# Kernel optimization log

Measured on AMD Instinct MI355X. Metric: run time of the kernel, lower is better.

Reference implementation:

```python
import jax, jax.numpy as jnp
import numpy as np

B, S, HID = 2, 2048, 2048
H, G = 16, 1
D = HID // H  # 128


def setup_inputs() -> dict:
    key = jax.random.key(0)
    ks = jax.random.split(key, 10)
    sc = 0.02
    inp = {
        "hidden_states": jax.random.normal(ks[0], (B, S, HID), jnp.float32),
        # 1 above the diagonal -> masked out (matches torch code: scores += mask * -1e9)
        "causal_mask": jnp.triu(jnp.ones((1, 1, S, S), jnp.float32), k=1),
        "padding_mask": jnp.zeros((B, S), jnp.float32),
        "Wq": jax.random.normal(ks[1], (HID, HID), jnp.float32) * sc,
        "bq": jnp.zeros((HID,), jnp.float32),
        "Wk": jax.random.normal(ks[2], (G * D, HID), jnp.float32) * sc,
        "bk": jnp.zeros((G * D,), jnp.float32),
        "Wv": jax.random.normal(ks[3], (G * D, HID), jnp.float32) * sc,
        "bv": jnp.zeros((G * D,), jnp.float32),
        "Wo": jax.random.normal(ks[4], (HID, HID), jnp.float32) * sc,
        "bo": jnp.zeros((HID,), jnp.float32),
    }
    return inp


def reference(hidden_states, causal_mask, padding_mask, Wq, bq, Wk, bk, Wv, bv, Wo, bo):
    b, s, _ = hidden_states.shape
    q = hidden_states @ Wq.T + bq            # [B,S,HID]
    k = hidden_states @ Wk.T + bk            # [B,S,G*D]
    v = hidden_states @ Wv.T + bv            # [B,S,G*D]
    q = q.reshape(b, s, H, D).transpose(0, 2, 1, 3)   # [B,H,S,D]
    k = k.reshape(b, s, G, D).transpose(0, 2, 1, 3)   # [B,G,S,D]
    v = v.reshape(b, s, G, D).transpose(0, 2, 1, 3)   # [B,G,S,D]
    # broadcast G=1 KV heads against H query heads (exactly what torch.matmul does)
    scores = jnp.matmul(q, jnp.swapaxes(k, -1, -2)) / jnp.sqrt(jnp.float32(D))  # [B,H,S,S]
    scores = scores + causal_mask * (-1e9)
    scores = scores + padding_mask[:, None, None, :] * (-1e9)
    weights = jax.nn.softmax(scores, axis=-1)
    out = jnp.matmul(weights, v)                       # [B,H,S,D]
    out = out.transpose(0, 2, 1, 3).reshape(b, s, H * D)
    return out @ Wo.T + bo
```

## Files before the change

kernel.cpp:

```cpp
#include <hip/hip_runtime.h>
#include <hip/hip_bf16.h>

typedef __attribute__((ext_vector_type(8))) short s8v;
typedef __attribute__((ext_vector_type(4))) float f4v;
typedef __hip_bfloat16 bf16;

#define S_LEN 2048
#define HID_DIM 2048
#define N_HEADS 16
#define HEAD_D 128
#define M_ROWS 4096
#define N_FUSED 2304

#define EXP2F(x) __builtin_amdgcn_exp2f(x)

typedef const __attribute__((address_space(1))) unsigned gu_t;
typedef __attribute__((address_space(3))) unsigned lu_t;

static __device__ inline void gload_lds16(const bf16* g, bf16* l) {
  __builtin_amdgcn_global_load_lds((gu_t*)(const void*)g, (lu_t*)(void*)l, 16, 0, 0);
}

static __device__ inline short f2b_bits(float f) {
  bf16 h = __float2bfloat16(f);
  short u;
  __builtin_memcpy(&u, &h, 2);
  return u;
}
static __device__ inline unsigned pk_bf16(float a, float b) {
  __hip_bfloat162 h2 = __float22bfloat162_rn(float2{a, b});
  unsigned u;
  __builtin_memcpy(&u, &h2, 4);
  return u;
}

struct Cvt5 {
  const float* src[5];
  bf16* dst[5];
  long n8[5];
};

__global__ __launch_bounds__(256) void cvt_f32_bf16(Cvt5 c) {
  long i = (long)blockIdx.x * 256 + threadIdx.x;
#pragma unroll
  for (int s = 0; s < 5; ++s) {
    long n8 = c.n8[s];
    if (i < n8) {
      const float* p = c.src[s] + i * 8;
      float4 f0 = *(const float4*)p;
      float4 f1 = *(const float4*)(p + 4);
      s8v t;
      t[0] = f2b_bits(f0.x); t[1] = f2b_bits(f0.y);
      t[2] = f2b_bits(f0.z); t[3] = f2b_bits(f0.w);
      t[4] = f2b_bits(f1.x); t[5] = f2b_bits(f1.y);
      t[6] = f2b_bits(f1.z); t[7] = f2b_bits(f1.w);
      *(s8v*)(c.dst[s] + i * 8) = t;
      return;
    }
    i -= n8;
  }
}

__global__ __launch_bounds__(256) void gemm_qkv(
    const bf16* __restrict__ A, const bf16* __restrict__ Wf,
    const float* __restrict__ bq, const float* __restrict__ bk,
    const float* __restrict__ bv,
    bf16* __restrict__ qout, bf16* __restrict__ kout, bf16* __restrict__ vtout) {
  __shared__ __align__(16) bf16 As[128 * 64];
  __shared__ __align__(16) bf16 Bs[128 * 64];
  const int t = threadIdx.x;
  const int lane = t & 63, wid = t >> 6;
  const int l15 = lane & 15, quad = lane >> 4;
  const int wm = wid >> 1, wn = wid & 1;
  const int bm = blockIdx.x, bn = blockIdx.y;
  const int lr = lane >> 3;
  const int lc = (lane & 7) * 8;
  f4v acc[4][4] = {};
  for (int kt = 0; kt < HID_DIM / 64; ++kt) {
    __syncthreads();
#pragma unroll
    for (int i = 0; i < 4; ++i) {
      int r0 = wid * 32 + i * 8;
      gload_lds16(&A[(size_t)(bm * 128 + r0 + lr) * HID_DIM + kt * 64 + lc], &As[r0 * 64]);
      gload_lds16(&Wf[(size_t)(bn * 128 + r0 + lr) * HID_DIM + kt * 64 + lc], &Bs[r0 * 64]);
    }
    __syncthreads();
#pragma unroll
    for (int ks = 0; ks < 2; ++ks) {
      s8v af[4], bfr[4];
#pragma unroll
      for (int mi = 0; mi < 4; ++mi)
        af[mi] = *(const s8v*)&As[(wm * 64 + mi * 16 + l15) * 64 + ks * 32 + quad * 8];
#pragma unroll
      for (int ni = 0; ni < 4; ++ni)
        bfr[ni] = *(const s8v*)&Bs[(wn * 64 + ni * 16 + l15) * 64 + ks * 32 + quad * 8];
#pragma unroll
      for (int mi = 0; mi < 4; ++mi)
#pragma unroll
        for (int ni = 0; ni < 4; ++ni)
          acc[mi][ni] = __builtin_amdgcn_mfma_f32_16x16x32_bf16(af[mi], bfr[ni], acc[mi][ni], 0, 0, 0);
    }
  }
  if (bn < 16) {
#pragma unroll
    for (int ni = 0; ni < 4; ++ni) {
      int cl = wn * 64 + ni * 16 + l15;
      float bvv = bq[bn * 128 + cl];
#pragma unroll
      for (int mi = 0; mi < 4; ++mi)
#pragma unroll
        for (int r = 0; r < 4; ++r) {
          int row = bm * 128 + wm * 64 + mi * 16 + quad * 4 + r;
          qout[(size_t)row * HID_DIM + bn * 128 + cl] = __float2bfloat16(acc[mi][ni][r] + bvv);
        }
    }
  } else if (bn == 16) {
#pragma unroll
    for (int ni = 0; ni < 4; ++ni) {
      int cl = wn * 64 + ni * 16 + l15;
      float bvv = bk[cl];
#pragma unroll
      for (int mi = 0; mi < 4; ++mi)
#pragma unroll
        for (int r = 0; r < 4; ++r) {
          int row = bm * 128 + wm * 64 + mi * 16 + quad * 4 + r;
          kout[(size_t)row * HEAD_D + cl] = __float2bfloat16(acc[mi][ni][r] + bvv);
        }
    }
  } else {
#pragma unroll
    for (int ni = 0; ni < 4; ++ni) {
      int cl = wn * 64 + ni * 16 + l15;
      float bvv = bv[cl];
#pragma unroll
      for (int mi = 0; mi < 4; ++mi)
#pragma unroll
        for (int r = 0; r < 4; ++r) {
          int row = bm * 128 + wm * 64 + mi * 16 + quad * 4 + r;
          vtout[(size_t)cl * M_ROWS + row] = __float2bfloat16(acc[mi][ni][r] + bvv);
        }
    }
  }
}

template <bool WBF>
__global__ __launch_bounds__(256) void gemm_o(
    const bf16* __restrict__ A, const void* __restrict__ Wp,
    const float* __restrict__ bias, float* __restrict__ C) {
  __shared__ __align__(16) bf16 As[128 * 64];
  __shared__ __align__(16) bf16 Bs[128 * 64];
  const int t = threadIdx.x;
  const int lane = t & 63, wid = t >> 6;
  const int l15 = lane & 15, quad = lane >> 4;
  const int wm = wid >> 1, wn = wid & 1;
  const int bm = blockIdx.x, bn = blockIdx.y;
  const int lr = lane >> 3;
  const int lc = (lane & 7) * 8;
  f4v acc[4][4] = {};
  for (int kt = 0; kt < HID_DIM / 64; ++kt) {
    __syncthreads();
#pragma unroll
    for (int i = 0; i < 4; ++i) {
      int r0 = wid * 32 + i * 8;
      gload_lds16(&A[(size_t)(bm * 128 + r0 + lr) * HID_DIM + kt * 64 + lc], &As[r0 * 64]);
      if constexpr (WBF) {
        gload_lds16(&((const bf16*)Wp)[(size_t)(bn * 128 + r0 + lr) * HID_DIM + kt * 64 + lc],
                    &Bs[r0 * 64]);
      }
    }
    if constexpr (!WBF) {
#pragma unroll
      for (int i = 0; i < 4; ++i) {
        int idx = t + i * 256;
        int row = idx >> 3, c8 = (idx & 7) * 8;
        const float* s = (const float*)Wp + (size_t)(bn * 128 + row) * HID_DIM + kt * 64 + c8;
        float4 f0 = *(const float4*)s;
        float4 f1 = *(const float4*)(s + 4);
        s8v tmp;
        tmp[0] = f2b_bits(f0.x); tmp[1] = f2b_bits(f0.y);
        tmp[2] = f2b_bits(f0.z); tmp[3] = f2b_bits(f0.w);
        tmp[4] = f2b_bits(f1.x); tmp[5] = f2b_bits(f1.y);
        tmp[6] = f2b_bits(f1.z); tmp[7] = f2b_bits(f1.w);
        *(s8v*)&Bs[row * 64 + c8] = tmp;
      }
    }
    __syncthreads();
#pragma unroll
    for (int ks = 0; ks < 2; ++ks) {
      s8v af[4], bfr[4];
#pragma unroll
      for (int mi = 0; mi < 4; ++mi)
        af[mi] = *(const s8v*)&As[(wm * 64 + mi * 16 + l15) * 64 + ks * 32 + quad * 8];
#pragma unroll
      for (int ni = 0; ni < 4; ++ni)
        bfr[ni] = *(const s8v*)&Bs[(wn * 64 + ni * 16 + l15) * 64 + ks * 32 + quad * 8];
#pragma unroll
      for (int mi = 0; mi < 4; ++mi)
#pragma unroll
        for (int ni = 0; ni < 4; ++ni)
          acc[mi][ni] = __builtin_amdgcn_mfma_f32_16x16x32_bf16(af[mi], bfr[ni], acc[mi][ni], 0, 0, 0);
    }
  }
#pragma unroll
  for (int ni = 0; ni < 4; ++ni) {
    int col = bn * 128 + wn * 64 + ni * 16 + l15;
    float bvv = bias[col];
#pragma unroll
    for (int mi = 0; mi < 4; ++mi)
#pragma unroll
      for (int r = 0; r < 4; ++r) {
        int row = bm * 128 + wm * 64 + mi * 16 + quad * 4 + r;
        C[(size_t)row * HID_DIM + col] = acc[mi][ni][r] + bvv;
      }
  }
}

__global__ __launch_bounds__(512, 2) void attn_fwd(
    const bf16* q, const bf16* __restrict__ k, const bf16* __restrict__ vt,
    bf16* o) {
  constexpr int FS = 528;
  __shared__ __align__(16) bf16 KsF[32 * FS];
  __shared__ __align__(16) bf16 VtF[32 * FS];
  __shared__ __align__(16) bf16 PsF[32 * FS];
  const int t = threadIdx.x;
  const int lane = t & 63, w = t >> 6;
  const int l15 = lane & 15, quad = lane >> 4;
  const int p = blockIdx.x >> 1, b = blockIdx.x & 1;
  const size_t bs = (size_t)b * S_LEN;
  const float scale2 = 0.12754245f;

  for (int cc = 0; cc < 2; ++cc) {
    const int c = cc ? p : (255 - p);
    const int row0 = c * 8;
    const int jt = (c >> 4) + 1;
    const int head = w * 2 + (l15 >> 3);

    s8v qf[4];
#pragma unroll
    for (int ks = 0; ks < 4; ++ks)
      qf[ks] = *(const s8v*)&q[(bs + row0 + (l15 & 7)) * HID_DIM +
                               head * HEAD_D + ks * 32 + quad * 8];

    float mst = -1e30f;
    float lst = 0.f;
    f4v acco[8] = {};

    uint4 kreg[4], vreg[4];
#pragma unroll
    for (int i = 0; i < 4; ++i) {
      int idx = t + i * 512;
      kreg[i] = *(const uint4*)&k[(bs + (idx >> 4)) * HEAD_D + (idx & 15) * 8];
      vreg[i] = *(const uint4*)&vt[(size_t)(idx >> 4) * M_ROWS + bs + (idx & 15) * 8];
    }

    for (int j = 0; j < jt; ++j) {
      __syncthreads();
#pragma unroll
      for (int i = 0; i < 4; ++i) {
        int idx = t + i * 512;
        int krow = idx >> 4, kc = idx & 15;
        *(uint4*)&KsF[(((krow >> 4) << 2) | (kc >> 2)) * FS + ((krow & 15) << 5) + ((kc & 3) << 3)] = kreg[i];
        *(uint4*)&VtF[(((krow >> 4) << 2) | (kc >> 2)) * FS + ((krow & 15) << 5) + ((kc & 3) << 3)] = vreg[i];
      }
      if (j + 1 < jt) {
#pragma unroll
        for (int i = 0; i < 4; ++i) {
          int idx = t + i * 512;
          kreg[i] = *(const uint4*)&k[(bs + (j + 1) * 128 + (idx >> 4)) * HEAD_D + (idx & 15) * 8];
          vreg[i] = *(const uint4*)&vt[(size_t)(idx >> 4) * M_ROWS + bs + (j + 1) * 128 + (idx & 15) * 8];
        }
      }
      __syncthreads();

      f4v accs[8] = {};
#pragma unroll
      for (int ks = 0; ks < 4; ++ks) {
        s8v kf[8];
#pragma unroll
        for (int ni = 0; ni < 8; ++ni)
          kf[ni] = *(const s8v*)&KsF[(ni * 4 + ks) * FS + l15 * 32 + quad * 8];
#pragma unroll
        for (int ni = 0; ni < 8; ++ni)
          accs[ni] = __builtin_amdgcn_mfma_f32_16x16x32_bf16(kf[ni], qf[ks], accs[ni], 0, 0, 0);
      }

      const int mg = row0 + (l15 & 7);
      const bool full = (j * 128 + 127 <= row0);
      float tmax = -1e30f;
#pragma unroll
      for (int ni = 0; ni < 8; ++ni)
#pragma unroll
        for (int r = 0; r < 4; ++r) {
          int ng = j * 128 + ni * 16 + quad * 4 + r;
          float s = accs[ni][r];
          if (!full && ng > mg) s = -1e30f;
          accs[ni][r] = s;
          tmax = fmaxf(tmax, s);
        }
      tmax = fmaxf(tmax, __shfl_xor(tmax, 16, 64));
      tmax = fmaxf(tmax, __shfl_xor(tmax, 32, 64));
      float mnew = fmaxf(mst, tmax);
      float nms = -mnew * scale2;
      float alpha = EXP2F(fmaf(mst, scale2, nms));
      float psum = 0.f;
#pragma unroll
      for (int ni = 0; ni < 8; ++ni) {
        float p0 = EXP2F(fmaf(accs[ni][0], scale2, nms));
        float p1 = EXP2F(fmaf(accs[ni][1], scale2, nms));
        float p2 = EXP2F(fmaf(accs[ni][2], scale2, nms));
        float p3 = EXP2F(fmaf(accs[ni][3], scale2, nms));
        psum += (p0 + p1) + (p2 + p3);
        uint2 packed;
        packed.x = pk_bf16(p0, p1);
        packed.y = pk_bf16(p2, p3);
        *(uint2*)&PsF[(w * 4 + (ni >> 1)) * FS + l15 * 32 + (ni & 1) * 16 + quad * 4] = packed;
      }
      psum += __shfl_xor(psum, 16, 64);
      psum += __shfl_xor(psum, 32, 64);
      lst = lst * alpha + psum;
      mst = mnew;
#pragma unroll
      for (int r = 0; r < 4; ++r) {
        float ar = __shfl(alpha, quad * 4 + r, 64);
#pragma unroll
        for (int di = 0; di < 8; ++di) acco[di][r] *= ar;
      }

#pragma unroll
      for (int ks = 0; ks < 4; ++ks) {
        s8v pf, vf[8];
        pf = *(const s8v*)&PsF[(w * 4 + ks) * FS + l15 * 32 + quad * 8];
#pragma unroll
        for (int di = 0; di < 8; ++di)
          vf[di] = *(const s8v*)&VtF[(di * 4 + ks) * FS + l15 * 32 + quad * 8];
#pragma unroll
        for (int di = 0; di < 8; ++di)
          acco[di] = __builtin_amdgcn_mfma_f32_16x16x32_bf16(pf, vf[di], acco[di], 0, 0, 0);
      }
    }

#pragma unroll
    for (int r = 0; r < 4; ++r) {
      int vmq = quad * 4 + r;
      float lr2 = __shfl(lst, vmq, 64);
      float rinv = 1.0f / lr2;
      size_t row = bs + row0 + (vmq & 7);
      int hd = w * 2 + (vmq >> 3);
#pragma unroll
      for (int di = 0; di < 8; ++di)
        o[row * HID_DIM + hd * HEAD_D + di * 16 + l15] = __float2bfloat16(acco[di][r] * rinv);
    }
  }
}

extern "C" void kernel_launch(void* const* d_in, const int* in_sizes, int n_in,
                              void* d_out, int out_size, void* d_ws, size_t ws_size,
                              hipStream_t stream) {
  const float* hs = (const float*)d_in[0];
  const float* Wq = (const float*)d_in[3];
  const float* bq = (const float*)d_in[4];
  const float* Wk = (const float*)d_in[5];
  const float* bk = (const float*)d_in[6];
  const float* Wv = (const float*)d_in[7];
  const float* bv = (const float*)d_in[8];
  const float* Wo = (const float*)d_in[9];
  const float* bo = (const float*)d_in[10];
  float* out = (float*)d_out;

  bf16* qab = (bf16*)d_ws;
  const bool big_ws = ws_size >= (size_t)25 * 1024 * 1024;
  bf16* wob = (bf16*)((char*)d_ws + (size_t)16 * 1024 * 1024);

  char* ob = (char*)d_out;
  bf16* kb = (bf16*)ob;
  bf16* vtb = (bf16*)(ob + (size_t)1048576);
  bf16* hsb = (bf16*)(ob + (size_t)2097152);
  bf16* wqkvb = (bf16*)(ob + (size_t)18874368);

  Cvt5 c;
  c.src[0] = hs; c.dst[0] = hsb;
  c.n8[0] = (long)M_ROWS * HID_DIM / 8;
  c.src[1] = Wq; c.dst[1] = wqkvb;
  c.n8[1] = (long)HID_DIM * HID_DIM / 8;
  c.src[2] = Wk; c.dst[2] = wqkvb + (size_t)HID_DIM * HID_DIM;
  c.n8[2] = (long)HEAD_D * HID_DIM / 8;
  c.src[3] = Wv; c.dst[3] = wqkvb + (size_t)(HID_DIM + HEAD_D) * HID_DIM;
  c.n8[3] = (long)HEAD_D * HID_DIM / 8;
  c.src[4] = Wo; c.dst[4] = big_ws ? wob : (bf16*)nullptr;
  c.n8[4] = big_ws ? (long)HID_DIM * HID_DIM / 8 : 0;
  long total8 = c.n8[0] + c.n8[1] + c.n8[2] + c.n8[3] + c.n8[4];

  cvt_f32_bf16<<<dim3((unsigned)((total8 + 255) / 256)), dim3(256), 0, stream>>>(c);
  gemm_qkv<<<dim3(M_ROWS / 128, N_FUSED / 128), dim3(256), 0, stream>>>(
      hsb, wqkvb, bq, bk, bv, qab, kb, vtb);
  attn_fwd<<<dim3(256), dim3(512), 0, stream>>>(qab, kb, vtb, qab);
  if (big_ws)
    gemm_o<true><<<dim3(M_ROWS / 128, HID_DIM / 128), dim3(256), 0, stream>>>(qab, wob, bo, out);
  else
    gemm_o<false><<<dim3(M_ROWS / 128, HID_DIM / 128), dim3(256), 0, stream>>>(qab, Wo, bo, out);
}
```

Before: 378.0 us.

## Double-buffer GEMM LDS tiles and swizzle attention LDS fragments

The QKV and output-projection GEMMs now use double-buffered LDS tiles. The next K-tile's global-to-LDS loads are issued before computing on the current tile, with one barrier per iteration, and launch bounds request 2 blocks per CU. The attention kernel applies an XOR swizzle to its K, V and P LDS fragment layout to reduce bank conflicts on the 16-byte reads and writes. This doubles GEMM LDS use to 64KB per block, which may limit occupancy. The fp32-weight path of gemm_o stays single-buffered.

```diff
diff --git a/kernel.cpp b/kernel.cpp
--- a/kernel.cpp
+++ b/kernel.cpp
@@ -33,6 +33,8 @@
   __builtin_memcpy(&u, &h2, 4);
   return u;
 }
+
+static __device__ inline int fswz(int i) { return i ^ (((i >> 6) & 3) << 3); }
 
 struct Cvt5 {
   const float* src[5];
@@ -61,13 +63,105 @@
   }
 }
 
-__global__ __launch_bounds__(256) void gemm_qkv(
+__global__ __launch_bounds__(256, 2) void gemm_qkv(
     const bf16* __restrict__ A, const bf16* __restrict__ Wf,
     const float* __restrict__ bq, const float* __restrict__ bk,
     const float* __restrict__ bv,
     bf16* __restrict__ qout, bf16* __restrict__ kout, bf16* __restrict__ vtout) {
-  __shared__ __align__(16) bf16 As[128 * 64];
-  __shared__ __align__(16) bf16 Bs[128 * 64];
+  __shared__ __align__(16) bf16 As[2][128 * 64];
+  __shared__ __align__(16) bf16 Bs[2][128 * 64];
+  const int t = threadIdx.x;
+  const int lane = t & 63, wid = t >> 6;
+  const int l15 = lane & 15, quad = lane >> 4;
+  const int wm = wid >> 1, wn = wid & 1;
+  const int bm = blockIdx.x, bn = blockIdx.y;
+  const int lr = lane >> 3;
+  const int lc = (lane & 7) * 8;
+  const bf16* Ab = &A[(size_t)(bm * 128 + lr) * HID_DIM + lc];
+  const bf16* Bb = &Wf[(size_t)(bn * 128 + lr) * HID_DIM + lc];
+  f4v acc[4][4] = {};
+#pragma unroll
+  for (int i = 0; i < 4; ++i) {
+    int r0 = wid * 32 + i * 8;
+    gload_lds16(Ab + (size_t)r0 * HID_DIM, &As[0][r0 * 64]);
+    gload_lds16(Bb + (size_t)r0 * HID_DIM, &Bs[0][r0 * 64]);
+  }
+  __syncthreads();
+  for (int kt = 0; kt < HID_DIM / 64; ++kt) {
+    const int cur = kt & 1;
+    if (kt + 1 < HID_DIM / 64) {
+#pragma unroll
+      for (int i = 0; i < 4; ++i) {
+        int r0 = wid * 32 + i * 8;
+        gload_lds16(Ab + (size_t)r0 * HID_DIM + (kt + 1) * 64, &As[cur ^ 1][r0 * 64]);
+        gload_lds16(Bb + (size_t)r0 * HID_DIM + (kt + 1) * 64, &Bs[cur ^ 1][r0 * 64]);
+      }
+    }
+#pragma unroll
+    for (int ks = 0; ks < 2; ++ks) {
+      s8v af[4], bfr[4];
+#pragma unroll
+      for (int mi = 0; mi < 4; ++mi)
+        af[mi] = *(const s8v*)&As[cur][(wm * 64 + mi * 16 + l15) * 64 + ks * 32 + quad * 8];
+#pragma unroll
+      for (int ni = 0; ni < 4; ++ni)
+        bfr[ni] = *(const s8v*)&Bs[cur][(wn * 64 + ni * 16 + l15) * 64 + ks * 32 + quad * 8];
+#pragma unroll
+      for (int mi = 0; mi < 4; ++mi)
+#pragma unroll
+        for (int ni = 0; ni < 4; ++ni)
+          acc[mi][ni] = __builtin_amdgcn_mfma_f32_16x16x32_bf16(af[mi], bfr[ni], acc[mi][ni], 0, 0, 0);
+    }
+    __syncthreads();
+  }
+  if (bn < 16) {
+#pragma unroll
+    for (int ni = 0; ni < 4; ++ni) {
+      int cl = wn * 64 + ni * 16 + l15;
+      float bvv = bq[bn * 128 + cl];
+#pragma unroll
+      for (int mi = 0; mi < 4; ++mi)
+#pragma unroll
+        for (int r = 0; r < 4; ++r) {
+          int row = bm * 128 + wm * 64 + mi * 16 + quad * 4 + r;
+          qout[(size_t)row * HID_DIM + bn * 128 + cl] = __float2bfloat16(acc[mi][ni][r] + bvv);
+        }
+    }
+  } else if (bn == 16) {
+#pragma unroll
+    for (int ni = 0; ni < 4; ++ni) {
+      int cl = wn * 64 + ni * 16 + l15;
+      float bvv = bk[cl];
+#pragma unroll
+      for (int mi = 0; mi < 4; ++mi)
+#pragma unroll
+        for (int r = 0; r < 4; ++r) {
+          int row = bm * 128 + wm * 64 + mi * 16 + quad * 4 + r;
+          kout[(size_t)row * HEAD_D + cl] = __float2bfloat16(acc[mi][ni][r] + bvv);
+        }
+    }
+  } else {
+#pragma unroll
+    for (int ni = 0; ni < 4; ++ni) {
+      int cl = wn * 64 + ni * 16 + l15;
+      float bvv = bv[cl];
+#pragma unroll
+      for (int mi = 0; mi < 4; ++mi)
+#pragma unroll
+        for (int r = 0; r < 4; ++r) {
+          int row = bm * 128 + wm * 64 + mi * 16 + quad * 4 + r;
+          vtout[(size_t)cl * M_ROWS + row] = __float2bfloat16(acc[mi][ni][r] + bvv);
+        }
+    }
+  }
+}
+
+template <bool WBF>
+__global__ __launch_bounds__(256, 2) void gemm_o(
+    const bf16* __restrict__ A, const void* __restrict__ Wp,
+    const float* __restrict__ bias, float* __restrict__ C) {
+  __shared__ __align__(16) bf16 As[2][128 * 64];
+  __shared__ __align__(16) bf16 Bs[2][128 * 64];
   const int t = threadIdx.x;
   const int lane = t & 63, wid = t >> 6;
   const int l15 = lane & 15, quad = lane >> 4;
@@ -76,99 +170,51 @@
   const int lr = lane >> 3;
   const int lc = (lane & 7) * 8;
   f4v acc[4][4] = {};
-  for (int kt = 0; kt < HID_DIM / 64; ++kt) {
-    __syncthreads();
+  if constexpr (WBF) {
+    const bf16* Ab = &A[(size_t)(bm * 128 + lr) * HID_DIM + lc];
+    const bf16* Bb = &((const bf16*)Wp)[(size_t)(bn * 128 + lr) * HID_DIM + lc];
 #pragma unroll
     for (int i = 0; i < 4; ++i) {
       int r0 = wid * 32 + i * 8;
-      gload_lds16(&A[(size_t)(bm * 128 + r0 + lr) * HID_DIM + kt * 64 + lc], &As[r0 * 64]);
-      gload_lds16(&Wf[(size_t)(bn * 128 + r0 + lr) * HID_DIM + kt * 64 + lc], &Bs[r0 * 64]);
+      gload_lds16(Ab + (size_t)r0 * HID_DIM, &As[0][r0 * 64]);
+      gload_lds16(Bb + (size_t)r0 * HID_DIM, &Bs[0][r0 * 64]);
     }
     __syncthreads();
-#pragma unroll
-    for (int ks = 0; ks < 2; ++ks) {
-      s8v af[4], bfr[4];
-#pragma unroll
-      for (int mi = 0; mi < 4; ++mi)
-        af[mi] = *(const s8v*)&As[(wm * 64 + mi * 16 + l15) * 64 + ks * 32 + quad * 8];
-#pragma unroll
-      for (int ni = 0; ni < 4; ++ni)
-        bfr[ni] = *(const s8v*)&Bs[(wn * 64 + ni * 16 + l15) * 64 + ks * 32 + quad * 8];
-#pragma unroll
-      for (int mi = 0; mi < 4; ++mi)
+    for (int kt = 0; kt < HID_DIM / 64; ++kt) {
+      const int cur = kt & 1;
+      if (kt + 1 < HID_DIM / 64) {
+#pragma unroll
+        for (int i = 0; i < 4; ++i) {
+          int r0 = wid * 32 + i * 8;
+          gload_lds16(Ab + (size_t)r0 * HID_DIM + (kt + 1) * 64, &As[cur ^ 1][r0 * 64]);
+          gload_lds16(Bb + (size_t)r0 * HID_DIM + (kt + 1) * 64, &Bs[cur ^ 1][r0 * 64]);
+        }
+      }
+#pragma unroll
+      for (int ks = 0; ks < 2; ++ks) {
+        s8v af[4], bfr[4];
+#pragma unroll
+        for (int mi = 0; mi < 4; ++mi)
+          af[mi] = *(const s8v*)&As[cur][(wm * 64 + mi * 16 + l15) * 64 + ks * 32 + quad * 8];
 #pragma unroll
         for (int ni = 0; ni < 4; ++ni)
-          acc[mi][ni] = __builtin_amdgcn_mfma_f32_16x16x32_bf16(af[mi], bfr[ni], acc[mi][ni], 0, 0, 0);
-    }
-  }
-  if (bn < 16) {
-#pragma unroll
-    for (int ni = 0; ni < 4; ++ni) {
-      int cl = wn * 64 + ni * 16 + l15;
-      float bvv = bq[bn * 128 + cl];
-#pragma unroll
-      for (int mi = 0; mi < 4; ++mi)
-#pragma unroll
-        for (int r = 0; r < 4; ++r) {
-          int row = bm * 128 + wm * 64 + mi * 16 + quad * 4 + r;
-          qout[(size_t)row * HID_DIM + bn * 128 + cl] = __float2bfloat16(acc[mi][ni][r] + bvv);
-        }
-    }
-  } else if (bn == 16) {
-#pragma unroll
-    for (int ni = 0; ni < 4; ++ni) {
-      int cl = wn * 64 + ni * 16 + l15;
-      float bvv = bk[cl];
-#pragma unroll
-      for (int mi = 0; mi < 4; ++mi)
-#pragma unroll
-        for (int r = 0; r < 4; ++r) {
-          int row = bm * 128 + wm * 64 + mi * 16 + quad * 4 + r;
-          kout[(size_t)row * HEAD_D + cl] = __float2bfloat16(acc[mi][ni][r] + bvv);
-        }
+          bfr[ni] = *(const s8v*)&Bs[cur][(wn * 64 + ni * 16 + l15) * 64 + ks * 32 + quad * 8];
+#pragma unroll
+        for (int mi = 0; mi < 4; ++mi)
+#pragma unroll
+          for (int ni = 0; ni < 4; ++ni)
+            acc[mi][ni] = __builtin_amdgcn_mfma_f32_16x16x32_bf16(af[mi], bfr[ni], acc[mi][ni], 0, 0, 0);
+      }
+      __syncthreads();
     }
   } else {
-#pragma unroll
-    for (int ni = 0; ni < 4; ++ni) {
-      int cl = wn * 64 + ni * 16 + l15;
-      float bvv = bv[cl];
-#pragma unroll
-      for (int mi = 0; mi < 4; ++mi)
-#pragma unroll
-        for (int r = 0; r < 4; ++r) {
-          int row = bm * 128 + wm * 64 + mi * 16 + quad * 4 + r;
-          vtout[(size_t)cl * M_ROWS + row] = __float2bfloat16(acc[mi][ni][r] + bvv);
-        }
-    }
-  }
-}
-
-template <bool WBF>
-__global__ __launch_bounds__(256) void gemm_o(
-    const bf16* __restrict__ A, const void* __restrict__ Wp,
-    const float* __restrict__ bias, float* __restrict__ C) {
-  __shared__ __align__(16) bf16 As[128 * 64];
-  __shared__ __align__(16) bf16 Bs[128 * 64];
-  const int t = threadIdx.x;
-  const int lane = t & 63, wid = t >> 6;
-  const int l15 = lane & 15, quad = lane >> 4;
-  const int wm = wid >> 1, wn = wid & 1;
-  const int bm = blockIdx.x, bn = blockIdx.y;
-  const int lr = lane >> 3;
-  const int lc = (lane & 7) * 8;
-  f4v acc[4][4] = {};
-  for (int kt = 0; kt < HID_DIM / 64; ++kt) {
-    __syncthreads();
-#pragma unroll
-    for (int i = 0; i < 4; ++i) {
-      int r0 = wid * 32 + i * 8;
-      gload_lds16(&A[(size_t)(bm * 128 + r0 + lr) * HID_DIM + kt * 64 + lc], &As[r0 * 64]);
-      if constexpr (WBF) {
-        gload_lds16(&((const bf16*)Wp)[(size_t)(bn * 128 + r0 + lr) * HID_DIM + kt * 64 + lc],
-                    &Bs[r0 * 64]);
-      }
-    }
-    if constexpr (!WBF) {
+    for (int kt = 0; kt < HID_DIM / 64; ++kt) {
+      __syncthreads();
+#pragma unroll
+      for (int i = 0; i < 4; ++i) {
+        int r0 = wid * 32 + i * 8;
+        gload_lds16(&A[(size_t)(bm * 128 + r0 + lr) * HID_DIM + kt * 64 + lc], &As[0][r0 * 64]);
+      }
 #pragma unroll
       for (int i = 0; i < 4; ++i) {
         int idx = t + i * 256;
@@ -181,24 +227,24 @@
         tmp[2] = f2b_bits(f0.z); tmp[3] = f2b_bits(f0.w);
         tmp[4] = f2b_bits(f1.x); tmp[5] = f2b_bits(f1.y);
         tmp[6] = f2b_bits(f1.z); tmp[7] = f2b_bits(f1.w);
-        *(s8v*)&Bs[row * 64 + c8] = tmp;
-      }
-    }
-    __syncthreads();
-#pragma unroll
-    for (int ks = 0; ks < 2; ++ks) {
-      s8v af[4], bfr[4];
-#pragma unroll
-      for (int mi = 0; mi < 4; ++mi)
-        af[mi] = *(const s8v*)&As[(wm * 64 + mi * 16 + l15) * 64 + ks * 32 + quad * 8];
-#pragma unroll
-      for (int ni = 0; ni < 4; ++ni)
-        bfr[ni] = *(const s8v*)&Bs[(wn * 64 + ni * 16 + l15) * 64 + ks * 32 + quad * 8];
-#pragma unroll
-      for (int mi = 0; mi < 4; ++mi)
+        *(s8v*)&Bs[0][row * 64 + c8] = tmp;
+      }
+      __syncthreads();
+#pragma unroll
+      for (int ks = 0; ks < 2; ++ks) {
+        s8v af[4], bfr[4];
+#pragma unroll
+        for (int mi = 0; mi < 4; ++mi)
+          af[mi] = *(const s8v*)&As[0][(wm * 64 + mi * 16 + l15) * 64 + ks * 32 + quad * 8];
 #pragma unroll
         for (int ni = 0; ni < 4; ++ni)
-          acc[mi][ni] = __builtin_amdgcn_mfma_f32_16x16x32_bf16(af[mi], bfr[ni], acc[mi][ni], 0, 0, 0);
+          bfr[ni] = *(const s8v*)&Bs[0][(wn * 64 + ni * 16 + l15) * 64 + ks * 32 + quad * 8];
+#pragma unroll
+        for (int mi = 0; mi < 4; ++mi)
+#pragma unroll
+          for (int ni = 0; ni < 4; ++ni)
+            acc[mi][ni] = __builtin_amdgcn_mfma_f32_16x16x32_bf16(af[mi], bfr[ni], acc[mi][ni], 0, 0, 0);
+      }
     }
   }
 #pragma unroll
@@ -259,8 +305,10 @@
       for (int i = 0; i < 4; ++i) {
         int idx = t + i * 512;
         int krow = idx >> 4, kc = idx & 15;
-        *(uint4*)&KsF[(((krow >> 4) << 2) | (kc >> 2)) * FS + ((krow & 15) << 5) + ((kc & 3) << 3)] = kreg[i];
-        *(uint4*)&VtF[(((krow >> 4) << 2) | (kc >> 2)) * FS + ((krow & 15) << 5) + ((kc & 3) << 3)] = vreg[i];
+        int frag = ((krow >> 4) << 2) | (kc >> 2);
+        int intr = fswz(((krow & 15) << 5) + ((kc & 3) << 3));
+        *(uint4*)&KsF[frag * FS + intr] = kreg[i];
+        *(uint4*)&VtF[frag * FS + intr] = vreg[i];
       }
       if (j + 1 < jt) {
 #pragma unroll
@@ -272,13 +320,14 @@
       }
       __syncthreads();
 
+      const int rdi = fswz(l15 * 32 + quad * 8);
       f4v accs[8] = {};
 #pragma unroll
       for (int ks = 0; ks < 4; ++ks) {
         s8v kf[8];
 #pragma unroll
         for (int ni = 0; ni < 8; ++ni)
-          kf[ni] = *(const s8v*)&KsF[(ni * 4 + ks) * FS + l15 * 32 + quad * 8];
+          kf[ni] = *(const s8v*)&KsF[(ni * 4 + ks) * FS + rdi];
 #pragma unroll
         for (int ni = 0; ni < 8; ++ni)
           accs[ni] = __builtin_amdgcn_mfma_f32_16x16x32_bf16(kf[ni], qf[ks], accs[ni], 0, 0, 0);
@@ -313,7 +362,8 @@
         uint2 packed;
         packed.x = pk_bf16(p0, p1);
         packed.y = pk_bf16(p2, p3);
-        *(uint2*)&PsF[(w * 4 + (ni >> 1)) * FS + l15 * 32 + (ni & 1) * 16 + quad * 4] = packed;
+        *(uint2*)&PsF[(w * 4 + (ni >> 1)) * FS +
+                      fswz(l15 * 32 + (ni & 1) * 16 + quad * 4)] = packed;
       }
       psum += __shfl_xor(psum, 16, 64);
       psum += __shfl_xor(psum, 32, 64);
@@ -329,10 +379,10 @@
 #pragma unroll
       for (int ks = 0; ks < 4; ++ks) {
         s8v pf, vf[8];
-        pf = *(const s8v*)&PsF[(w * 4 + ks) * FS + l15 * 32 + quad * 8];
+        pf = *(const s8v*)&PsF[(w * 4 + ks) * FS + rdi];
 #pragma unroll
         for (int di = 0; di < 8; ++di)
-          vf[di] = *(const s8v*)&VtF[(di * 4 + ks) * FS + l15 * 32 + quad * 8];
+          vf[di] = *(const s8v*)&VtF[(di * 4 + ks) * FS + rdi];
 #pragma unroll
         for (int di = 0; di < 8; ++di)
           acco[di] = __builtin_amdgcn_mfma_f32_16x16x32_bf16(pf, vf[di], acco[di], 0, 0, 0);
```

Measured after the change: 396.4 us. 4.9% more time.
